# Kernel tuning notes

Hardware: AMD Instinct MI355X
Metric: run time of the kernel (lower is better)

## Reference

```python
import jax, jax.numpy as jnp
import numpy as np

H, KV, HD, HID = 32, 8, 128, 4096
THETA, FACTOR, HI_FF, LO_FF, ORIG_MAX = 500000.0, 8.0, 4.0, 1.0, 8192


def _llama3_inv_freq():
    # standard Llama-3 rope scaling
    inv = 1.0 / (THETA ** (np.arange(0, HD, 2, dtype=np.float64) / HD))
    wavelen = 2.0 * np.pi / inv
    low_wl = ORIG_MAX / LO_FF
    high_wl = ORIG_MAX / HI_FF
    smooth = (ORIG_MAX / wavelen - LO_FF) / (HI_FF - LO_FF)
    scaled = np.where(wavelen > low_wl, inv / FACTOR, inv)
    mid = (wavelen <= low_wl) & (wavelen >= high_wl)
    scaled = np.where(mid, (1 - smooth) * inv / FACTOR + smooth * inv, scaled)
    return scaled.astype(np.float32)


def _rope_cos_sin(T):
    inv = _llama3_inv_freq()                       # [HD/2]
    pos = np.arange(T, dtype=np.float32)
    freqs = pos[:, None] * inv[None, :]            # [T, HD/2]
    emb = np.concatenate([freqs, freqs], axis=-1)  # [T, HD]
    return jnp.asarray(np.cos(emb)), jnp.asarray(np.sin(emb))


def _rotate_half(x):
    x1, x2 = jnp.split(x, 2, axis=-1)
    return jnp.concatenate([-x2, x1], axis=-1)


def setup_inputs() -> dict:
    key = jax.random.key(0)
    ks = jax.random.split(key, 5)
    s = 1.0 / np.sqrt(HID)
    return {
        "x": jax.random.normal(ks[0], (1, 2048, HID), jnp.float32),
        "wq": jax.random.normal(ks[1], (HID, H * HD), jnp.float32) * s,
        "wk": jax.random.normal(ks[2], (HID, KV * HD), jnp.float32) * s,
        "wv": jax.random.normal(ks[3], (HID, KV * HD), jnp.float32) * s,
        "wo": jax.random.normal(ks[4], (H * HD, HID), jnp.float32) * s,
    }


def reference(x, wq, wk, wv, wo):
    B, T, _ = x.shape
    q = (x @ wq).reshape(B, T, H, HD).transpose(0, 2, 1, 3)   # [B,H,T,D]
    k = (x @ wk).reshape(B, T, KV, HD).transpose(0, 2, 1, 3)  # [B,KV,T,D]
    v = (x @ wv).reshape(B, T, KV, HD).transpose(0, 2, 1, 3)
    cos, sin = _rope_cos_sin(T)                               # [T,D]
    q = q * cos + _rotate_half(q) * sin
    k = k * cos + _rotate_half(k) * sin
    rep = H // KV
    k = jnp.repeat(k, rep, axis=1)                            # [B,H,T,D]
    v = jnp.repeat(v, rep, axis=1)
    scores = jnp.einsum("bhtd,bhsd->bhts", q, k) * (1.0 / np.sqrt(HD))
    mask = jnp.tril(jnp.ones((T, T), dtype=bool))
    scores = jnp.where(mask, scores, -jnp.inf)
    att = jax.nn.softmax(scores, axis=-1)
    out = jnp.einsum("bhts,bhsd->bhtd", att, v)
    out = out.transpose(0, 2, 1, 3).reshape(B, T, H * HD)
    return out @ wo
```

## Files before the change

### kernel.cpp

```cpp
#include <hip/hip_runtime.h>
#include <math.h>

#define T_SEQ 2048
#define HID   4096
#define NH    32
#define NKV   8
#define HD    128
#define QCOLS (NH*HD)
#define KCOLS (NKV*HD)
#define KSTR  2048

typedef _Float16 f16;
typedef _Float16 f16x8 __attribute__((ext_vector_type(8)));
typedef _Float16 f16x4 __attribute__((ext_vector_type(4)));
typedef float f32x4 __attribute__((ext_vector_type(4)));

#define GLDS(g, l) __builtin_amdgcn_global_load_lds( \
    (const __attribute__((address_space(1))) void*)(g), \
    (__attribute__((address_space(3))) void*)(l), 16, 0, 0)

__global__ void rope_table(float* __restrict__ cosT, float* __restrict__ sinT) {
    int idx = blockIdx.x * blockDim.x + threadIdx.x;
    if (idx >= T_SEQ * 64) return;
    int t = idx >> 6, i = idx & 63;
    double inv = pow(500000.0, -(double)(2 * i) / 128.0);
    double wavelen = 6.283185307179586 / inv;
    const double lowwl = 8192.0, highwl = 2048.0;
    double scaled;
    if (wavelen > lowwl) {
        scaled = inv / 8.0;
    } else if (wavelen >= highwl) {
        double smooth = (8192.0 / wavelen - 1.0) / 3.0;
        scaled = (1.0 - smooth) * inv / 8.0 + smooth * inv;
    } else {
        scaled = inv;
    }
    float invf = (float)scaled;
    float phase = (float)t * invf;
    cosT[idx] = (float)cos((double)phase);
    sinT[idx] = (float)sin((double)phase);
}

__global__ void convert_f32_f16(const float* __restrict__ in, f16* __restrict__ out, int n8) {
    int i = blockIdx.x * blockDim.x + threadIdx.x;
    if (i >= n8) return;
    float4 a = *(const float4*)(in + (size_t)i * 8);
    float4 b = *(const float4*)(in + (size_t)i * 8 + 4);
    f16x8 v = {(f16)a.x, (f16)a.y, (f16)a.z, (f16)a.w, (f16)b.x, (f16)b.y, (f16)b.z, (f16)b.w};
    *(f16x8*)(out + (size_t)i * 8) = v;
}

__global__ __launch_bounds__(256) void transpose_f32_to_f16(const float* __restrict__ in,
                                                            f16* __restrict__ out,
                                                            int R, int ld) {
    __shared__ f16 t[64][72];
    const int tid = threadIdx.x;
    const int r0 = blockIdx.y * 64, c0 = blockIdx.x * 64;
#pragma unroll
    for (int i = 0; i < 4; ++i) {
        int r = i * 16 + (tid >> 4), c4 = (tid & 15) * 4;
        float4 v = *(const float4*)(in + (size_t)(r0 + r) * ld + c0 + c4);
        t[r][c4 + 0] = (f16)v.x; t[r][c4 + 1] = (f16)v.y;
        t[r][c4 + 2] = (f16)v.z; t[r][c4 + 3] = (f16)v.w;
    }
    __syncthreads();
    int n = tid >> 2, j0 = (tid & 3) * 16;
    f16x8 a, b;
#pragma unroll
    for (int j = 0; j < 8; ++j) { a[j] = t[j0 + j][n]; b[j] = t[j0 + 8 + j][n]; }
    *(f16x8*)(out + (size_t)(c0 + n) * R + r0 + j0) = a;
    *(f16x8*)(out + (size_t)(c0 + n) * R + r0 + j0 + 8) = b;
}

__global__ __launch_bounds__(256) void transpose_f16(const f16* __restrict__ in,
                                                     f16* __restrict__ out,
                                                     int R, int ld) {
    __shared__ f16 t[64][72];
    const int tid = threadIdx.x;
    const int r0 = blockIdx.y * 64, c0 = blockIdx.x * 64;
#pragma unroll
    for (int i = 0; i < 2; ++i) {
        int r = i * 32 + (tid >> 3), c8 = (tid & 7) * 8;
        f16x8 v = *(const f16x8*)(in + (size_t)(r0 + r) * ld + c0 + c8);
#pragma unroll
        for (int j = 0; j < 8; ++j) t[r][c8 + j] = v[j];
    }
    __syncthreads();
    int n = tid >> 2, j0 = (tid & 3) * 16;
    f16x8 a, b;
#pragma unroll
    for (int j = 0; j < 8; ++j) { a[j] = t[j0 + j][n]; b[j] = t[j0 + 8 + j][n]; }
    *(f16x8*)(out + (size_t)(c0 + n) * R + r0 + j0) = a;
    *(f16x8*)(out + (size_t)(c0 + n) * R + r0 + j0 + 8) = b;
}

template <typename OutT>
__global__ __launch_bounds__(256, 2) void gemm_f16(const f16* __restrict__ A,
                                                   const f16* __restrict__ Bt,
                                                   OutT* __restrict__ C,
                                                   int M, int ldc, int K) {
    __shared__ f16 As[2][128 * 64];
    __shared__ f16 Bs[2][128 * 64];
    const int tid = threadIdx.x;
    const int l = tid & 63;
    const int w = tid >> 6, wr = w >> 1, wc = w & 1;
    const int c16 = l & 15, g = l >> 4;
    const int m0 = blockIdx.y * 128, n0 = blockIdx.x * 128;

    f32x4 acc[4][4] = {};

    const int r_src = tid >> 3;
    const int colswz = ((tid & 7) * 8) ^ ((r_src & 7) << 3);
    const f16* gA = A + (size_t)(m0 + r_src) * K + colswz;
    const f16* gB = Bt + (size_t)(n0 + r_src) * K + colswz;

    auto stage = [&](f16* sA, f16* sB, int k0) {
#pragma unroll
        for (int i = 0; i < 4; ++i) {
            GLDS(gA + (size_t)(i * 32) * K + k0, sA + i * 2048 + tid * 8);
            GLDS(gB + (size_t)(i * 32) * K + k0, sB + i * 2048 + tid * 8);
        }
    };
    auto compute = [&](const f16* sA, const f16* sB) {
#pragma unroll
        for (int kk = 0; kk < 2; ++kk) {
            f16x8 af[4], bf[4];
#pragma unroll
            for (int mb = 0; mb < 4; ++mb) {
                int row = wr * 64 + mb * 16 + c16;
                af[mb] = *(const f16x8*)((const char*)sA + row * 128 +
                                         ((kk * 64 + g * 16) ^ ((row & 7) << 4)));
            }
#pragma unroll
            for (int nb = 0; nb < 4; ++nb) {
                int row = wc * 64 + nb * 16 + c16;
                bf[nb] = *(const f16x8*)((const char*)sB + row * 128 +
                                         ((kk * 64 + g * 16) ^ ((row & 7) << 4)));
            }
#pragma unroll
            for (int mb = 0; mb < 4; ++mb)
#pragma unroll
                for (int nb = 0; nb < 4; ++nb)
                    acc[mb][nb] = __builtin_amdgcn_mfma_f32_16x16x32_f16(af[mb], bf[nb], acc[mb][nb], 0, 0, 0);
        }
    };

    stage(As[0], Bs[0], 0);
    __syncthreads();
    int cur = 0;
    for (int k0 = 64; k0 < K; k0 += 64) {
        stage(As[cur ^ 1], Bs[cur ^ 1], k0);
        compute(As[cur], Bs[cur]);
        __syncthreads();
        cur ^= 1;
    }
    compute(As[cur], Bs[cur]);

#pragma unroll
    for (int mb = 0; mb < 4; ++mb)
#pragma unroll
        for (int nb = 0; nb < 4; ++nb)
#pragma unroll
            for (int r = 0; r < 4; ++r) {
                size_t row = m0 + wr * 64 + mb * 16 + g * 4 + r;
                C[row * ldc + n0 + wc * 64 + nb * 16 + c16] = (OutT)acc[mb][nb][r];
            }
}

__global__ void rope_apply_f16(f16* __restrict__ data, const float* __restrict__ cosT,
                               const float* __restrict__ sinT, int nheads, int stride) {
    int idx = blockIdx.x * blockDim.x + threadIdx.x;
    int lane = idx & 63;
    int row = idx >> 6;
    if (row >= T_SEQ * nheads) return;
    int t = row / nheads, h = row % nheads;
    f16* p = data + (size_t)t * stride + h * HD;
    float c = cosT[t * 64 + lane], s = sinT[t * 64 + lane];
    float x1 = (float)p[lane], x2 = (float)p[lane + 64];
    p[lane]      = (f16)(x1 * c - x2 * s);
    p[lane + 64] = (f16)(x2 * c + x1 * s);
}

__global__ __launch_bounds__(256, 3) void attn_f16(const f16* __restrict__ q,
                                                   const f16* __restrict__ k,
                                                   const f16* __restrict__ vt,
                                                   f16* __restrict__ outh) {
    __shared__ f16 Ks[64 * 128];
    __shared__ f16 Vs[128 * 64];
    __shared__ f16 Ps[4][16 * 72];
    const int tid = threadIdx.x;
    const int l = tid & 63, w = tid >> 6;
    const int c16 = l & 15, g = l >> 4;
    const int h = blockIdx.y, kvh = h >> 2;
    const float SCALE = 0.08838834764831845f;

    for (int pass = 0; pass < 2; ++pass) {
        const int qt = pass ? 31 - (int)blockIdx.x : (int)blockIdx.x;
        const int qrow = qt * 64 + w * 16 + c16;

        f16x8 qf[4];
        const f16* qbase = q + (size_t)qrow * QCOLS + h * HD;
#pragma unroll
        for (int ks = 0; ks < 4; ++ks) qf[ks] = *(const f16x8*)(qbase + ks * 32 + g * 8);

        f32x4 o[8] = {};
        float mrun = -INFINITY, lrun = 0.f;

        for (int ch = 0; ch <= qt; ++ch) {
            __syncthreads();
            {
                const char* kg = (const char*)(k + (size_t)(ch * 64) * KSTR + kvh * HD);
                int r = tid >> 2;
#pragma unroll
                for (int i = 0; i < 4; ++i) {
                    int b = (tid & 3) * 16 + i * 64;
                    uint4 d = *(const uint4*)(kg + (size_t)r * (KSTR * 2) + b);
                    *(uint4*)((char*)Ks + r * 256 + (b ^ ((r & 7) << 4))) = d;
                }
                const char* vg = (const char*)(vt + (size_t)(kvh * HD) * T_SEQ + ch * 64);
                int d2 = tid >> 1;
#pragma unroll
                for (int i = 0; i < 4; ++i) {
                    int b = (tid & 1) * 16 + i * 32;
                    uint4 dd = *(const uint4*)(vg + (size_t)d2 * (T_SEQ * 2) + b);
                    *(uint4*)((char*)Vs + d2 * 128 + (b ^ ((d2 & 7) << 4))) = dd;
                }
            }
            __syncthreads();

            f32x4 st[4];
            __builtin_amdgcn_s_setprio(1);
#pragma unroll
            for (int kb = 0; kb < 4; ++kb) {
                f32x4 a = {};
#pragma unroll
                for (int ks = 0; ks < 4; ++ks) {
                    int row = kb * 16 + c16;
                    f16x8 kf = *(const f16x8*)((const char*)Ks + row * 256 +
                                               ((ks * 64 + g * 16) ^ ((row & 7) << 4)));
                    a = __builtin_amdgcn_mfma_f32_16x16x32_f16(kf, qf[ks], a, 0, 0, 0);
                }
                st[kb] = a;
            }
            __builtin_amdgcn_s_setprio(0);

            float p[16];
            float cmax = -INFINITY;
            const bool diag = (ch == qt);
#pragma unroll
            for (int kb = 0; kb < 4; ++kb)
#pragma unroll
                for (int r = 0; r < 4; ++r) {
                    float s = st[kb][r] * SCALE;
                    if (diag) {
                        int key = ch * 64 + kb * 16 + g * 4 + r;
                        if (key > qrow) s = -INFINITY;
                    }
                    p[kb * 4 + r] = s;
                    cmax = fmaxf(cmax, s);
                }
            cmax = fmaxf(cmax, __shfl_xor(cmax, 16));
            cmax = fmaxf(cmax, __shfl_xor(cmax, 32));
            float mnew = fmaxf(mrun, cmax);
            float corr = __expf(mrun - mnew);
            float psum = 0.f;
#pragma unroll
            for (int i = 0; i < 16; ++i) { float e = __expf(p[i] - mnew); p[i] = e; psum += e; }
            psum += __shfl_xor(psum, 16);
            psum += __shfl_xor(psum, 32);
            lrun = lrun * corr + psum;
            mrun = mnew;
#pragma unroll
            for (int mb = 0; mb < 8; ++mb) o[mb] *= corr;

            f16* pw = Ps[w] + c16 * 72;
#pragma unroll
            for (int kb = 0; kb < 4; ++kb) {
                f16x4 q4 = {(f16)p[kb * 4], (f16)p[kb * 4 + 1], (f16)p[kb * 4 + 2], (f16)p[kb * 4 + 3]};
                *(f16x4*)(pw + kb * 16 + g * 4) = q4;
            }

            __builtin_amdgcn_s_setprio(1);
#pragma unroll
            for (int ks2 = 0; ks2 < 2; ++ks2) {
                f16x8 pf = *(const f16x8*)(Ps[w] + c16 * 72 + ks2 * 32 + g * 8);
#pragma unroll
                for (int mb = 0; mb < 8; ++mb) {
                    int row = mb * 16 + c16;
                    f16x8 vf = *(const f16x8*)((const char*)Vs + row * 128 +
                                               ((ks2 * 64 + g * 16) ^ ((row & 7) << 4)));
                    o[mb] = __builtin_amdgcn_mfma_f32_16x16x32_f16(vf, pf, o[mb], 0, 0, 0);
                }
            }
            __builtin_amdgcn_s_setprio(0);
        }

        float invl = 1.f / lrun;
        f16* ob = outh + (size_t)qrow * QCOLS + h * HD;
#pragma unroll
        for (int mb = 0; mb < 8; ++mb) {
            f16x4 v = {(f16)(o[mb][0] * invl), (f16)(o[mb][1] * invl),
                       (f16)(o[mb][2] * invl), (f16)(o[mb][3] * invl)};
            *(f16x4*)(ob + mb * 16 + g * 4) = v;
        }
    }
}

extern "C" void kernel_launch(void* const* d_in, const int* in_sizes, int n_in,
                              void* d_out, int out_size, void* d_ws, size_t ws_size,
                              hipStream_t stream) {
    const float* x  = (const float*)d_in[0];
    const float* wq = (const float*)d_in[1];
    const float* wk = (const float*)d_in[2];
    const float* wv = (const float*)d_in[3];
    const float* wo = (const float*)d_in[4];
    float* out = (float*)d_out;

    char* ws = (char*)d_ws;
    const size_t MB = 1024ULL * 1024ULL;
    float* cosT = (float*)(ws);
    float* sinT = (float*)(ws + 512 * 1024ULL);
    f16* xh   = (f16*)(ws + 1 * MB);
    f16* atth = xh;
    f16* qh   = (f16*)(ws + 17 * MB);
    f16* kvh  = (f16*)(ws + 33 * MB);
    f16* wT   = (f16*)(ws + 41 * MB);
    f16* vtb  = (f16*)(ws + 73 * MB);

    rope_table<<<dim3((T_SEQ * 64 + 255) / 256), dim3(256), 0, stream>>>(cosT, sinT);
    convert_f32_f16<<<dim3(T_SEQ * HID / 8 / 256), dim3(256), 0, stream>>>(x, xh, T_SEQ * HID / 8);

    transpose_f32_to_f16<<<dim3(QCOLS / 64, HID / 64), dim3(256), 0, stream>>>(wq, wT, HID, QCOLS);
    gemm_f16<f16><<<dim3(QCOLS / 128, T_SEQ / 128), dim3(256), 0, stream>>>(
        xh, wT, qh, T_SEQ, QCOLS, HID);

    transpose_f32_to_f16<<<dim3(KCOLS / 64, HID / 64), dim3(256), 0, stream>>>(wk, wT, HID, KCOLS);
    transpose_f32_to_f16<<<dim3(KCOLS / 64, HID / 64), dim3(256), 0, stream>>>(
        wv, wT + (size_t)KCOLS * HID, HID, KCOLS);
    gemm_f16<f16><<<dim3(KSTR / 128, T_SEQ / 128), dim3(256), 0, stream>>>(
        xh, wT, kvh, T_SEQ, KSTR, HID);

    rope_apply_f16<<<dim3(T_SEQ * NH * 64 / 256), dim3(256), 0, stream>>>(
        qh, cosT, sinT, NH, QCOLS);
    rope_apply_f16<<<dim3(T_SEQ * NKV * 64 / 256), dim3(256), 0, stream>>>(
        kvh, cosT, sinT, NKV, KSTR);

    transpose_f16<<<dim3(KCOLS / 64, T_SEQ / 64), dim3(256), 0, stream>>>(
        kvh + KCOLS, vtb, T_SEQ, KSTR);

    attn_f16<<<dim3(16, NH), dim3(256), 0, stream>>>(qh, kvh, vtb, atth);

    transpose_f32_to_f16<<<dim3(HID / 64, QCOLS / 64), dim3(256), 0, stream>>>(wo, wT, QCOLS, HID);
    gemm_f16<float><<<dim3(HID / 128, T_SEQ / 128), dim3(256), 0, stream>>>(
        atth, wT, out, T_SEQ, HID, QCOLS);
}
```

Before: 363.4 us.

## Double-buffer K/V via global_load_lds and share tiles across both query tiles

Restructures the causal attention kernel so each block processes its two paired query tiles together, loading each K/V chunk once and reusing it for both. K/V chunks are double-buffered in LDS using asynchronous global-to-LDS loads, so the next chunk's loads overlap the current chunk's compute and one barrier per iteration is removed. This doubles LDS use and raises register pressure from two accumulator sets, so launch bounds drop from 3 to 2 blocks per CU.

```diff
diff --git a/kernel.cpp b/kernel.cpp
--- a/kernel.cpp
+++ b/kernel.cpp
@@ -181,128 +181,145 @@
     p[lane + 64] = (f16)(x2 * c + x1 * s);
 }
 
-__global__ __launch_bounds__(256, 3) void attn_f16(const f16* __restrict__ q,
+__global__ __launch_bounds__(256, 2) void attn_f16(const f16* __restrict__ q,
                                                    const f16* __restrict__ k,
                                                    const f16* __restrict__ vt,
                                                    f16* __restrict__ outh) {
-    __shared__ f16 Ks[64 * 128];
-    __shared__ f16 Vs[128 * 64];
+    __shared__ f16 Ks[2][64 * 128];
+    __shared__ f16 Vs[2][128 * 64];
     __shared__ f16 Ps[4][16 * 72];
     const int tid = threadIdx.x;
     const int l = tid & 63, w = tid >> 6;
     const int c16 = l & 15, g = l >> 4;
-    const int h = blockIdx.y, kvh = h >> 2;
+    const int bx = blockIdx.x, h = blockIdx.y, kvh = h >> 2;
+    const int qtA = bx, qtB = 31 - bx;
     const float SCALE = 0.08838834764831845f;
 
-    for (int pass = 0; pass < 2; ++pass) {
-        const int qt = pass ? 31 - (int)blockIdx.x : (int)blockIdx.x;
-        const int qrow = qt * 64 + w * 16 + c16;
-
-        f16x8 qf[4];
-        const f16* qbase = q + (size_t)qrow * QCOLS + h * HD;
-#pragma unroll
-        for (int ks = 0; ks < 4; ++ks) qf[ks] = *(const f16x8*)(qbase + ks * 32 + g * 8);
-
-        f32x4 o[8] = {};
-        float mrun = -INFINITY, lrun = 0.f;
-
-        for (int ch = 0; ch <= qt; ++ch) {
-            __syncthreads();
-            {
-                const char* kg = (const char*)(k + (size_t)(ch * 64) * KSTR + kvh * HD);
-                int r = tid >> 2;
-#pragma unroll
-                for (int i = 0; i < 4; ++i) {
-                    int b = (tid & 3) * 16 + i * 64;
-                    uint4 d = *(const uint4*)(kg + (size_t)r * (KSTR * 2) + b);
-                    *(uint4*)((char*)Ks + r * 256 + (b ^ ((r & 7) << 4))) = d;
+    const int qrowA = qtA * 64 + w * 16 + c16;
+    const int qrowB = qtB * 64 + w * 16 + c16;
+
+    f16x8 qfA[4], qfB[4];
+    {
+        const f16* qa = q + (size_t)qrowA * QCOLS + h * HD;
+        const f16* qb = q + (size_t)qrowB * QCOLS + h * HD;
+#pragma unroll
+        for (int ks = 0; ks < 4; ++ks) {
+            qfA[ks] = *(const f16x8*)(qa + ks * 32 + g * 8);
+            qfB[ks] = *(const f16x8*)(qb + ks * 32 + g * 8);
+        }
+    }
+
+    f32x4 oA[8] = {}, oB[8] = {};
+    float mA = -INFINITY, lA = 0.f, mB = -INFINITY, lB = 0.f;
+
+    const int kr = tid >> 4, kboff = (tid & 15) * 16;
+    const int vr = tid >> 3, vboff = (tid & 7) * 16;
+    const char* kgb = (const char*)(k + kvh * HD);
+    const char* vgb = (const char*)(vt + (size_t)(kvh * HD) * T_SEQ);
+
+    auto stage = [&](int buf, int ch) {
+#pragma unroll
+        for (int i = 0; i < 4; ++i) {
+            int r = i * 16 + kr;
+            GLDS(kgb + (size_t)(ch * 64 + r) * (KSTR * 2) + (kboff ^ ((r & 7) << 4)),
+                 (char*)Ks[buf] + i * 4096 + tid * 16);
+            int d = i * 32 + vr;
+            GLDS(vgb + (size_t)d * (T_SEQ * 2) + (size_t)(ch * 64) * 2 + (vboff ^ ((d & 7) << 4)),
+                 (char*)Vs[buf] + i * 4096 + tid * 16);
+        }
+    };
+
+    auto compute = [&](int buf, const f16x8 (&qf)[4], f32x4 (&o)[8],
+                       float& mrun, float& lrun, int qrow, bool diag, int ch) {
+        f32x4 st[4];
+        __builtin_amdgcn_s_setprio(1);
+#pragma unroll
+        for (int kb = 0; kb < 4; ++kb) {
+            f32x4 a = {};
+#pragma unroll
+            for (int ks = 0; ks < 4; ++ks) {
+                int row = kb * 16 + c16;
+                f16x8 kf = *(const f16x8*)((const char*)Ks[buf] + row * 256 +
+                                           ((ks * 64 + g * 16) ^ ((row & 7) << 4)));
+                a = __builtin_amdgcn_mfma_f32_16x16x32_f16(kf, qf[ks], a, 0, 0, 0);
+            }
+            st[kb] = a;
+        }
+        __builtin_amdgcn_s_setprio(0);
+
+        float p[16];
+        float cmax = -INFINITY;
+#pragma unroll
+        for (int kb = 0; kb < 4; ++kb)
+#pragma unroll
+            for (int r = 0; r < 4; ++r) {
+                float s = st[kb][r] * SCALE;
+                if (diag) {
+                    int key = ch * 64 + kb * 16 + g * 4 + r;
+                    if (key > qrow) s = -INFINITY;
                 }
-                const char* vg = (const char*)(vt + (size_t)(kvh * HD) * T_SEQ + ch * 64);
-                int d2 = tid >> 1;
-#pragma unroll
-                for (int i = 0; i < 4; ++i) {
-                    int b = (tid & 1) * 16 + i * 32;
-                    uint4 dd = *(const uint4*)(vg + (size_t)d2 * (T_SEQ * 2) + b);
-                    *(uint4*)((char*)Vs + d2 * 128 + (b ^ ((d2 & 7) << 4))) = dd;
-                }
-            }
-            __syncthreads();
-
-            f32x4 st[4];
-            __builtin_amdgcn_s_setprio(1);
-#pragma unroll
-            for (int kb = 0; kb < 4; ++kb) {
-                f32x4 a = {};
-#pragma unroll
-                for (int ks = 0; ks < 4; ++ks) {
-                    int row = kb * 16 + c16;
-                    f16x8 kf = *(const f16x8*)((const char*)Ks + row * 256 +
-                                               ((ks * 64 + g * 16) ^ ((row & 7) << 4)));
-                    a = __builtin_amdgcn_mfma_f32_16x16x32_f16(kf, qf[ks], a, 0, 0, 0);
-                }
-                st[kb] = a;
-            }
-            __builtin_amdgcn_s_setprio(0);
-
-            float p[16];
-            float cmax = -INFINITY;
-            const bool diag = (ch == qt);
-#pragma unroll
-            for (int kb = 0; kb < 4; ++kb)
-#pragma unroll
-                for (int r = 0; r < 4; ++r) {
-                    float s = st[kb][r] * SCALE;
-                    if (diag) {
-                        int key = ch * 64 + kb * 16 + g * 4 + r;
-                        if (key > qrow) s = -INFINITY;
-                    }
-                    p[kb * 4 + r] = s;
-                    cmax = fmaxf(cmax, s);
-                }
-            cmax = fmaxf(cmax, __shfl_xor(cmax, 16));
-            cmax = fmaxf(cmax, __shfl_xor(cmax, 32));
-            float mnew = fmaxf(mrun, cmax);
-            float corr = __expf(mrun - mnew);
-            float psum = 0.f;
-#pragma unroll
-            for (int i = 0; i < 16; ++i) { float e = __expf(p[i] - mnew); p[i] = e; psum += e; }
-            psum += __shfl_xor(psum, 16);
-            psum += __shfl_xor(psum, 32);
-            lrun = lrun * corr + psum;
-            mrun = mnew;
-#pragma unroll
-            for (int mb = 0; mb < 8; ++mb) o[mb] *= corr;
-
-            f16* pw = Ps[w] + c16 * 72;
-#pragma unroll
-            for (int kb = 0; kb < 4; ++kb) {
-                f16x4 q4 = {(f16)p[kb * 4], (f16)p[kb * 4 + 1], (f16)p[kb * 4 + 2], (f16)p[kb * 4 + 3]};
-                *(f16x4*)(pw + kb * 16 + g * 4) = q4;
-            }
-
-            __builtin_amdgcn_s_setprio(1);
-#pragma unroll
-            for (int ks2 = 0; ks2 < 2; ++ks2) {
-                f16x8 pf = *(const f16x8*)(Ps[w] + c16 * 72 + ks2 * 32 + g * 8);
-#pragma unroll
-                for (int mb = 0; mb < 8; ++mb) {
-                    int row = mb * 16 + c16;
-                    f16x8 vf = *(const f16x8*)((const char*)Vs + row * 128 +
-                                               ((ks2 * 64 + g * 16) ^ ((row & 7) << 4)));
-                    o[mb] = __builtin_amdgcn_mfma_f32_16x16x32_f16(vf, pf, o[mb], 0, 0, 0);
-                }
-            }
-            __builtin_amdgcn_s_setprio(0);
-        }
-
-        float invl = 1.f / lrun;
-        f16* ob = outh + (size_t)qrow * QCOLS + h * HD;
-#pragma unroll
-        for (int mb = 0; mb < 8; ++mb) {
-            f16x4 v = {(f16)(o[mb][0] * invl), (f16)(o[mb][1] * invl),
-                       (f16)(o[mb][2] * invl), (f16)(o[mb][3] * invl)};
-            *(f16x4*)(ob + mb * 16 + g * 4) = v;
-        }
+                p[kb * 4 + r] = s;
+                cmax = fmaxf(cmax, s);
+            }
+        cmax = fmaxf(cmax, __shfl_xor(cmax, 16));
+        cmax = fmaxf(cmax, __shfl_xor(cmax, 32));
+        float mnew = fmaxf(mrun, cmax);
+        float corr = __expf(mrun - mnew);
+        float psum = 0.f;
+#pragma unroll
+        for (int i = 0; i < 16; ++i) { float e = __expf(p[i] - mnew); p[i] = e; psum += e; }
+        psum += __shfl_xor(psum, 16);
+        psum += __shfl_xor(psum, 32);
+        lrun = lrun * corr + psum;
+        mrun = mnew;
+#pragma unroll
+        for (int mb = 0; mb < 8; ++mb) o[mb] *= corr;
+
+        f16* pw = Ps[w] + c16 * 72;
+#pragma unroll
+        for (int kb = 0; kb < 4; ++kb) {
+            f16x4 q4 = {(f16)p[kb * 4], (f16)p[kb * 4 + 1], (f16)p[kb * 4 + 2], (f16)p[kb * 4 + 3]};
+            *(f16x4*)(pw + kb * 16 + g * 4) = q4;
+        }
+
+        __builtin_amdgcn_s_setprio(1);
+#pragma unroll
+        for (int ks2 = 0; ks2 < 2; ++ks2) {
+            f16x8 pf = *(const f16x8*)(Ps[w] + c16 * 72 + ks2 * 32 + g * 8);
+#pragma unroll
+            for (int mb = 0; mb < 8; ++mb) {
+                int row = mb * 16 + c16;
+                f16x8 vf = *(const f16x8*)((const char*)Vs[buf] + row * 128 +
+                                           ((ks2 * 64 + g * 16) ^ ((row & 7) << 4)));
+                o[mb] = __builtin_amdgcn_mfma_f32_16x16x32_f16(vf, pf, o[mb], 0, 0, 0);
+            }
+        }
+        __builtin_amdgcn_s_setprio(0);
+    };
+
+    stage(0, 0);
+    __syncthreads();
+    int cur = 0;
+    for (int ch = 0; ; ++ch) {
+        if (ch < qtB) stage(cur ^ 1, ch + 1);
+        compute(cur, qfB, oB, mB, lB, qrowB, ch == qtB, ch);
+        if (ch <= qtA) compute(cur, qfA, oA, mA, lA, qrowA, ch == qtA, ch);
+        if (ch == qtB) break;
+        __syncthreads();
+        cur ^= 1;
+    }
+
+    float ivA = 1.f / lA, ivB = 1.f / lB;
+    f16* oa = outh + (size_t)qrowA * QCOLS + h * HD;
+    f16* ob = outh + (size_t)qrowB * QCOLS + h * HD;
+#pragma unroll
+    for (int mb = 0; mb < 8; ++mb) {
+        f16x4 va = {(f16)(oA[mb][0] * ivA), (f16)(oA[mb][1] * ivA),
+                    (f16)(oA[mb][2] * ivA), (f16)(oA[mb][3] * ivA)};
+        f16x4 vb = {(f16)(oB[mb][0] * ivB), (f16)(oB[mb][1] * ivB),
+                    (f16)(oB[mb][2] * ivB), (f16)(oB[mb][3] * ivB)};
+        *(f16x4*)(oa + mb * 16 + g * 4) = va;
+        *(f16x4*)(ob + mb * 16 + g * 4) = vb;
     }
 }
 
```

After: 418.4 us. +15.1%, slower.
